# Optimization experiments

Hardware: AMD Instinct MI355X
Metric: run time of the kernel (lower is better)

The kernel has to match this reference:

```python
import jax, jax.numpy as jnp
import numpy as np

N = 50000   # nodes
E = 300000  # edges (before self-loops)
G = 64      # graphs in batch
F = 64      # feature_dim
H = 4       # n_head
C = 64      # per-head out channels (= feature_dim)
LAT = 256   # latent_dim
NEG_SLOPE = 0.2  # PyG GATConv default


def setup_inputs() -> dict:
    key = jax.random.key(0)
    ks = jax.random.split(key, 32)
    f32 = jnp.float32

    def w(k, shape, fan_in):
        return jax.random.normal(k, shape, dtype=f32) * (1.0 / np.sqrt(fan_in))

    return {
        "building_feature": jax.random.normal(ks[0], (N, 5), dtype=f32),
        "edge_index": jax.random.randint(ks[1], (2, E), 0, N, dtype=jnp.int32),
        "batch": jnp.sort(jax.random.randint(ks[2], (N,), 0, G, dtype=jnp.int32)),
        "bf_W": w(ks[3], (5, F), 5), "bf_b": jnp.zeros((F,), f32),
        "W1": w(ks[4], (F, H * C), F), "as1": w(ks[5], (H, C), C), "ad1": w(ks[6], (H, C), C), "b1": jnp.zeros((H * C,), f32),
        "W2": w(ks[7], (H * C, H * C), H * C), "as2": w(ks[8], (H, C), C), "ad2": w(ks[9], (H, C), C), "b2": jnp.zeros((H * C,), f32),
        "W3": w(ks[10], (H * C, H * C), H * C), "as3": w(ks[11], (H, C), C), "ad3": w(ks[12], (H, C), C), "b3": jnp.zeros((H * C,), f32),
        "agg_W": w(ks[13], (F * (1 + H * 3), LAT), F * (1 + H * 3)), "agg_b": jnp.zeros((LAT,), f32),
        "mu_W": w(ks[14], (LAT, LAT), LAT), "mu_b": jnp.zeros((LAT,), f32),
        "var_W": w(ks[15], (LAT, LAT), LAT), "var_b": jnp.zeros((LAT,), f32),
    }


def _gat_conv(x, W, att_src, att_dst, bias, src, dst):
    # PyG GATConv, concat=True, add_self_loops already in src/dst.
    h = (x @ W).reshape(-1, H, C)                       # [N,H,C]
    a_s = jnp.einsum("nhc,hc->nh", h, att_src)          # [N,H]
    a_d = jnp.einsum("nhc,hc->nh", h, att_dst)
    e = jax.nn.leaky_relu(a_s[src] + a_d[dst], NEG_SLOPE)  # [E,H]
    # segment softmax over incoming edges of each dst node
    m = jax.ops.segment_max(e, dst, num_segments=N)
    p = jnp.exp(e - m[dst])
    s = jax.ops.segment_sum(p, dst, num_segments=N)
    alpha = p / s[dst]                                  # [E,H]
    out = jax.ops.segment_sum(alpha[:, :, None] * h[src], dst, num_segments=N)
    return out.reshape(-1, H * C) + bias


def reference(building_feature, edge_index, batch,
              bf_W, bf_b,
              W1, as1, ad1, b1,
              W2, as2, ad2, b2,
              W3, as3, ad3, b3,
              agg_W, agg_b, mu_W, mu_b, var_W, var_b):
    # add self-loops (PyG GATConv default add_self_loops=True)
    loops = jnp.arange(N, dtype=edge_index.dtype)
    src = jnp.concatenate([edge_index[0], loops])
    dst = jnp.concatenate([edge_index[1], loops])

    n0 = jax.nn.relu(building_feature @ bf_W + bf_b)                 # [N,F]
    n1 = jax.nn.relu(_gat_conv(n0, W1, as1, ad1, b1, src, dst))      # [N,H*C]
    n2 = jax.nn.relu(_gat_conv(n1, W2, as2, ad2, b2, src, dst))
    n3 = jax.nn.relu(_gat_conv(n2, W3, as3, ad3, b3, src, dst))

    g = jnp.concatenate([
        jax.ops.segment_max(n0, batch, num_segments=G),
        jax.ops.segment_max(n1, batch, num_segments=G),
        jax.ops.segment_max(n2, batch, num_segments=G),
        jax.ops.segment_max(n3, batch, num_segments=G),
    ], axis=1)                                                       # [G, F*(1+3H)]

    latent = g @ agg_W + agg_b
    mu = latent @ mu_W + mu_b
    log_var = latent @ var_W + var_b
    return mu, log_var
```

## Files before the change

### kernel.cpp

```cpp
#include <hip/hip_runtime.h>
#include <hip/hip_bf16.h>

#define NN 50000
#define NPAD 50048
#define EE 300000
#define ETOT (EE + NN)
#define GG 64
#define GCOLS 832
#define LATD 256
#define BM 128
#define BN 128
#define NB_SCAN 196
#define LOG2E 1.4426950408889634f

typedef unsigned short u16;
typedef short s16x8 __attribute__((ext_vector_type(8)));
typedef float f32x4 __attribute__((ext_vector_type(4)));

__device__ __forceinline__ u16 f2bf(float f) {
    union { float f; unsigned u; } v; v.f = f;
    unsigned r = v.u + 0x7FFFu + ((v.u >> 16) & 1u);
    return (u16)(r >> 16);
}
__device__ __forceinline__ float bf2f(u16 u) {
    union { unsigned u; float f; } v; v.u = ((unsigned)u) << 16;
    return v.f;
}

__global__ __launch_bounds__(256) void k_prep(const float* __restrict__ W1, const float* __restrict__ W2,
                                              const float* __restrict__ W3, u16* __restrict__ Wt1,
                                              u16* __restrict__ Wt2, u16* __restrict__ Wt3,
                                              const float* __restrict__ bf, const float* __restrict__ Wb,
                                              const float* __restrict__ bb, const int* __restrict__ batch,
                                              u16* __restrict__ n0bf, int* __restrict__ gbuf,
                                              const int* __restrict__ ei, int* __restrict__ counts,
                                              u16* __restrict__ nbf) {
    int b = blockIdx.x;
    if (b < 576) {
        int idx = b * 256 + threadIdx.x;
        if (idx < 16384) {
            int n = idx >> 6, k = idx & 63;
            Wt1[idx] = f2bf(W1[k * 256 + n]);
        } else if (idx < 81920) {
            int t = idx - 16384; int n = t >> 8, k = t & 255;
            Wt2[t] = f2bf(W2[k * 256 + n]);
        } else {
            int t = idx - 81920; int n = t >> 8, k = t & 255;
            Wt3[t] = f2bf(W3[k * 256 + n]);
        }
    } else if (b < 967) {
        int c = threadIdx.x & 63;
        int sub = threadIdx.x >> 6;
        int base = (b - 576) * 128;
        int end = min(base + 128, NN);
        float w0 = Wb[c], w1 = Wb[64 + c], w2 = Wb[128 + c], w3 = Wb[192 + c], w4 = Wb[256 + c], bb_ = bb[c];
        float mx = 0.f;
        int curg = -1;
        for (int n = base + sub; n < end; n += 4) {
            const float* r = bf + (size_t)n * 5;
            float v = bb_ + r[0] * w0 + r[1] * w1 + r[2] * w2 + r[3] * w3 + r[4] * w4;
            v = fmaxf(v, 0.f);
            n0bf[(size_t)n * 64 + c] = f2bf(v);
            int g = batch[n];
            if (g != curg) {
                if (curg >= 0) atomicMax(&gbuf[curg * GCOLS + c], __float_as_int(mx));
                mx = 0.f; curg = g;
            }
            mx = fmaxf(mx, v);
        }
        if (curg >= 0) atomicMax(&gbuf[curg * GCOLS + c], __float_as_int(mx));
    } else if (b < 2335) {
        int e = (b - 967) * 256 + threadIdx.x;
        if (e < ETOT) {
            int d = (e < EE) ? ei[EE + e] : (e - EE);
            atomicAdd(&counts[d], 1);
        }
    } else {
        u16* p0 = n0bf + (size_t)NN * 64;
        for (int i = threadIdx.x; i < (NPAD - NN) * 64; i += 256) p0[i] = 0;
        u16* p1 = nbf + (size_t)NN * 256;
        for (int i = threadIdx.x; i < (NPAD - NN) * 256; i += 256) p1[i] = 0;
    }
}

__global__ __launch_bounds__(256) void k_scan_block(const int* __restrict__ counts, int* __restrict__ scanned,
                                                    int* __restrict__ bsums, int n) {
    __shared__ int sh[256];
    int i = blockIdx.x * 256 + threadIdx.x;
    int v = (i < n) ? counts[i] : 0;
    sh[threadIdx.x] = v; __syncthreads();
    for (int d = 1; d < 256; d <<= 1) {
        int t = (threadIdx.x >= d) ? sh[threadIdx.x - d] : 0;
        __syncthreads();
        sh[threadIdx.x] += t;
        __syncthreads();
    }
    if (i < n) scanned[i] = sh[threadIdx.x] - v;
    if (threadIdx.x == 255) bsums[blockIdx.x] = sh[255];
}

__global__ __launch_bounds__(256) void k_scan_add2(const int* __restrict__ scanned, const int* __restrict__ bsums,
                                                   int* __restrict__ indptr, int* __restrict__ fill) {
    __shared__ int sh[256];
    int t = threadIdx.x;
    int v = (t < NB_SCAN) ? bsums[t] : 0;
    sh[t] = v; __syncthreads();
    for (int d = 1; d < 256; d <<= 1) {
        int u = (t >= d) ? sh[t - d] : 0;
        __syncthreads();
        sh[t] += u;
        __syncthreads();
    }
    int bix = blockIdx.x;
    int boff = (bix == 0) ? 0 : sh[bix - 1];
    int i = bix * 256 + t;
    if (i < NN) { indptr[i] = scanned[i] + boff; fill[i] = 0; }
    if (i == 0) indptr[NN] = ETOT;
}

__global__ __launch_bounds__(256) void k_fill(const int* __restrict__ ei, const int* __restrict__ indptr,
                                              int* __restrict__ fill, int* __restrict__ esrc) {
    int e = blockIdx.x * 256 + threadIdx.x;
    if (e >= ETOT) return;
    int s, d;
    if (e < EE) { s = ei[e]; d = ei[EE + e]; } else { s = d = e - EE; }
    int pos = atomicAdd(&fill[d], 1);
    esrc[indptr[d] + pos] = s;
}

__global__ __launch_bounds__(256) void k_gemm_mfma(const u16* __restrict__ A,
                                                   const u16* __restrict__ Bt,
                                                   const float* __restrict__ att_s,
                                                   const float* __restrict__ att_d,
                                                   u16* __restrict__ Hbf,
                                                   float* __restrict__ a_s,
                                                   float* __restrict__ a_d,
                                                   int K) {
    __shared__ __align__(16) u16 As[128 * 64];
    __shared__ __align__(16) u16 Bs[128 * 64];
    const int tid = threadIdx.x;
    const int lane = tid & 63;
    const int w = tid >> 6;
    const int wr = w >> 1, wc = w & 1;
    const int row0 = blockIdx.x * BM;
    const int col0 = blockIdx.y * BN;

    f32x4 acc[4][4] = {};

    for (int kt = 0; kt < K; kt += 64) {
#pragma unroll
        for (int i = 0; i < 4; ++i) {
            int u = i * 256 + tid;
            int r = u >> 3, c16 = u & 7;
            int sc = ((c16 ^ (r & 7)) << 3);
            const u16* ga = A + (size_t)(row0 + r) * K + kt + sc;
            u16* la = &As[(size_t)(i * 256 + (w << 6)) * 8];
            __builtin_amdgcn_global_load_lds((const __attribute__((address_space(1))) void*)ga,
                                             (__attribute__((address_space(3))) void*)la, 16, 0, 0);
        }
#pragma unroll
        for (int i = 0; i < 4; ++i) {
            int u = i * 256 + tid;
            int r = u >> 3, c16 = u & 7;
            int sc = ((c16 ^ (r & 7)) << 3);
            const u16* gb = Bt + (size_t)(col0 + r) * K + kt + sc;
            u16* lb = &Bs[(size_t)(i * 256 + (w << 6)) * 8];
            __builtin_amdgcn_global_load_lds((const __attribute__((address_space(1))) void*)gb,
                                             (__attribute__((address_space(3))) void*)lb, 16, 0, 0);
        }
        __syncthreads();
#pragma unroll
        for (int ks = 0; ks < 2; ++ks) {
            s16x8 af[4], bfr[4];
#pragma unroll
            for (int m = 0; m < 4; ++m) {
                int ra = wr * 64 + m * 16 + (lane & 15);
                int c16 = ks * 4 + (lane >> 4);
                int off = ra * 64 + ((c16 ^ (ra & 7)) << 3);
                af[m] = *reinterpret_cast<const s16x8*>(&As[off]);
            }
#pragma unroll
            for (int n = 0; n < 4; ++n) {
                int rb = wc * 64 + n * 16 + (lane & 15);
                int c16 = ks * 4 + (lane >> 4);
                int off = rb * 64 + ((c16 ^ (rb & 7)) << 3);
                bfr[n] = *reinterpret_cast<const s16x8*>(&Bs[off]);
            }
#pragma unroll
            for (int m = 0; m < 4; ++m)
#pragma unroll
                for (int n = 0; n < 4; ++n)
                    acc[m][n] = __builtin_amdgcn_mfma_f32_16x16x32_bf16(af[m], bfr[n], acc[m][n], 0, 0, 0);
        }
        __syncthreads();
    }

    const int head = (blockIdx.y << 1) + wc;
    float asv[4], adv[4];
#pragma unroll
    for (int n = 0; n < 4; ++n) {
        asv[n] = att_s[head * 64 + n * 16 + (lane & 15)] * LOG2E;
        adv[n] = att_d[head * 64 + n * 16 + (lane & 15)] * LOG2E;
    }
#pragma unroll
    for (int m = 0; m < 4; ++m) {
        int growb = row0 + wr * 64 + m * 16 + (lane >> 4) * 4;
#pragma unroll
        for (int j = 0; j < 4; ++j) {
            int grow = growb + j;
            u16* orow = Hbf + (size_t)grow * 256 + col0 + wc * 64 + (lane & 15);
            float vs = 0.f, vd = 0.f;
#pragma unroll
            for (int n = 0; n < 4; ++n) {
                float v = acc[m][n][j];
                orow[n * 16] = f2bf(v);
                vs += v * asv[n];
                vd += v * adv[n];
            }
            vs += __shfl_xor(vs, 1); vd += __shfl_xor(vd, 1);
            vs += __shfl_xor(vs, 2); vd += __shfl_xor(vd, 2);
            vs += __shfl_xor(vs, 4); vd += __shfl_xor(vd, 4);
            vs += __shfl_xor(vs, 8); vd += __shfl_xor(vd, 8);
            if ((lane & 15) == 0) {
                a_s[grow * 4 + head] = vs;
                a_d[grow * 4 + head] = vd;
            }
        }
    }
}

__global__ __launch_bounds__(1024) void k_agg(const u16* __restrict__ Hbf, const float* __restrict__ a_s,
                                              const float* __restrict__ a_d, const int* __restrict__ indptr,
                                              const int* __restrict__ esrc, const float* __restrict__ bias,
                                              const int* __restrict__ batch, u16* __restrict__ outbf,
                                              int* __restrict__ gbuf, int poolOff) {
    __shared__ int lpool[2][256];
    if (threadIdx.x < 512) lpool[threadIdx.x >> 8][threadIdx.x & 255] = 0;
    __syncthreads();

    const int nodeBase = blockIdx.x * 16;
    const int wv = threadIdx.x >> 6;
    const int wid = nodeBase + wv;
    const int lane = threadIdx.x & 63;
    const int h = lane >> 4;
    const int eidx = lane & 15;
    const bool active = wid < NN;

    if (active) {
        int beg = indptr[wid];
        int dcount = indptr[wid + 1] - beg;
        float ad = a_d[wid * 4 + h];
        float mx = -3.0e38f, ssum = 0.f;
        float ax = 0.f, ay = 0.f, az = 0.f, aw = 0.f;

        for (int cb = 0; cb < dcount; cb += 16) {
            int cnt = min(16, dcount - cb);
            int s = (eidx < cnt) ? esrc[beg + cb + eidx] : 0;
            float el = (eidx < cnt) ? a_s[s * 4 + h] + ad : -3.0e38f;
            el = fmaxf(el, 0.2f * el);
            float cm = el;
            cm = fmaxf(cm, __shfl_xor(cm, 1));
            cm = fmaxf(cm, __shfl_xor(cm, 2));
            cm = fmaxf(cm, __shfl_xor(cm, 4));
            cm = fmaxf(cm, __shfl_xor(cm, 8));
            float nm = fmaxf(mx, cm);
            if (__any(nm > mx)) {
                float corr = exp2f(mx - nm);
                ssum *= corr; ax *= corr; ay *= corr; az *= corr; aw *= corr;
                mx = nm;
            }
            float p = exp2f(el - mx);
            float cs = p;
            cs += __shfl_xor(cs, 1);
            cs += __shfl_xor(cs, 2);
            cs += __shfl_xor(cs, 4);
            cs += __shfl_xor(cs, 8);
            ssum += cs;
            int e2 = 0;
            for (; e2 + 2 <= cnt; e2 += 2) {
                int s0 = __shfl(s, e2), s1 = __shfl(s, e2 + 1);
                float p0 = __shfl(p, (lane & 48) | e2);
                float p1 = __shfl(p, (lane & 48) | (e2 + 1));
                const ushort4 h0 = *reinterpret_cast<const ushort4*>(Hbf + (size_t)s0 * 256 + lane * 4);
                const ushort4 h1 = *reinterpret_cast<const ushort4*>(Hbf + (size_t)s1 * 256 + lane * 4);
                ax += p0 * bf2f(h0.x) + p1 * bf2f(h1.x);
                ay += p0 * bf2f(h0.y) + p1 * bf2f(h1.y);
                az += p0 * bf2f(h0.z) + p1 * bf2f(h1.z);
                aw += p0 * bf2f(h0.w) + p1 * bf2f(h1.w);
            }
            if (e2 < cnt) {
                int s0 = __shfl(s, e2);
                float p0 = __shfl(p, (lane & 48) | e2);
                const ushort4 h0 = *reinterpret_cast<const ushort4*>(Hbf + (size_t)s0 * 256 + lane * 4);
                ax += p0 * bf2f(h0.x);
                ay += p0 * bf2f(h0.y);
                az += p0 * bf2f(h0.z);
                aw += p0 * bf2f(h0.w);
            }
        }

        float inv = 1.0f / ssum;
        const float4 bv = *reinterpret_cast<const float4*>(bias + lane * 4);
        float o0 = fmaxf(ax * inv + bv.x, 0.f);
        float o1 = fmaxf(ay * inv + bv.y, 0.f);
        float o2 = fmaxf(az * inv + bv.z, 0.f);
        float o3 = fmaxf(aw * inv + bv.w, 0.f);
        ushort4 ob; ob.x = f2bf(o0); ob.y = f2bf(o1); ob.z = f2bf(o2); ob.w = f2bf(o3);
        *reinterpret_cast<ushort4*>(outbf + (size_t)wid * 256 + lane * 4) = ob;

        int g = batch[wid];
        int g0 = batch[nodeBase];
        int slot = g - g0;
        int c4 = lane * 4;
        if (slot < 2) {
            atomicMax(&lpool[slot][c4],     __float_as_int(o0));
            atomicMax(&lpool[slot][c4 + 1], __float_as_int(o1));
            atomicMax(&lpool[slot][c4 + 2], __float_as_int(o2));
            atomicMax(&lpool[slot][c4 + 3], __float_as_int(o3));
        } else {
            int* cell = &gbuf[g * GCOLS + poolOff + c4];
            atomicMax(cell,     __float_as_int(o0));
            atomicMax(cell + 1, __float_as_int(o1));
            atomicMax(cell + 2, __float_as_int(o2));
            atomicMax(cell + 3, __float_as_int(o3));
        }
    }
    __syncthreads();
    if (threadIdx.x < 512) {
        int slot = threadIdx.x >> 8, c = threadIdx.x & 255;
        int v = lpool[slot][c];
        if (v != 0) {
            int g0 = batch[nodeBase];
            atomicMax(&gbuf[(g0 + slot) * GCOLS + poolOff + c], v);
        }
    }
}

__global__ __launch_bounds__(1024) void k_head(const int* __restrict__ gbuf,
                                               const float* __restrict__ aggW, const float* __restrict__ aggb,
                                               const float* __restrict__ muW, const float* __restrict__ mub,
                                               const float* __restrict__ varW, const float* __restrict__ varb,
                                               float* __restrict__ out) {
    __shared__ float part[4][256];
    __shared__ float lat[LATD];
    int gi = blockIdx.x;
    int j = threadIdx.x & 255, ks = threadIdx.x >> 8;
    const float* g = (const float*)gbuf + (size_t)gi * GCOLS;
    float acc = 0.f;
    int k0 = ks * 208;
    for (int k = k0; k < k0 + 208; ++k) acc += g[k] * aggW[k * 256 + j];
    part[ks][j] = acc;
    __syncthreads();
    if (ks == 0) lat[j] = part[0][j] + part[1][j] + part[2][j] + part[3][j] + aggb[j];
    __syncthreads();
    const float* W = (ks < 2) ? muW : varW;
    int kb = (ks & 1) * 128;
    float am = 0.f;
    for (int k = kb; k < kb + 128; ++k) am += lat[k] * W[k * 256 + j];
    part[ks][j] = am;
    __syncthreads();
    if (ks == 0) out[(size_t)gi * 256 + j] = part[0][j] + part[1][j] + mub[j];
    else if (ks == 1) out[(size_t)GG * 256 + (size_t)gi * 256 + j] = part[2][j] + part[3][j] + varb[j];
}

extern "C" void kernel_launch(void* const* d_in, const int* in_sizes, int n_in,
                              void* d_out, int out_size, void* d_ws, size_t ws_size,
                              hipStream_t stream) {
    const float* bf   = (const float*)d_in[0];
    const int*   ei   = (const int*)d_in[1];
    const int*   batch= (const int*)d_in[2];
    const float* bf_W = (const float*)d_in[3];
    const float* bf_b = (const float*)d_in[4];
    const float* W1   = (const float*)d_in[5];
    const float* as1  = (const float*)d_in[6];
    const float* ad1  = (const float*)d_in[7];
    const float* b1   = (const float*)d_in[8];
    const float* W2   = (const float*)d_in[9];
    const float* as2  = (const float*)d_in[10];
    const float* ad2  = (const float*)d_in[11];
    const float* b2   = (const float*)d_in[12];
    const float* W3   = (const float*)d_in[13];
    const float* as3  = (const float*)d_in[14];
    const float* ad3  = (const float*)d_in[15];
    const float* b3   = (const float*)d_in[16];
    const float* aggW = (const float*)d_in[17];
    const float* aggb = (const float*)d_in[18];
    const float* muW  = (const float*)d_in[19];
    const float* mub  = (const float*)d_in[20];
    const float* varW = (const float*)d_in[21];
    const float* varb = (const float*)d_in[22];
    float* out = (float*)d_out;

    size_t off = 0;
    auto alloc = [&](size_t bytes) -> char* {
        char* p = (char*)d_ws + off;
        off += (bytes + 255) & ~(size_t)255;
        return p;
    };
    int*   counts  = (int*)alloc((size_t)(NN + GG * GCOLS) * 4);
    int*   gbuf    = counts + NN;
    u16*   Hbf     = (u16*)alloc((size_t)NPAD * 256 * 2);
    u16*   n0bf    = (u16*)alloc((size_t)NPAD * 64 * 2);
    u16*   nbf     = (u16*)alloc((size_t)NPAD * 256 * 2);
    float* a_s     = (float*)alloc((size_t)NPAD * 4 * 4);
    float* a_d     = (float*)alloc((size_t)NPAD * 4 * 4);
    int*   scanned = (int*)alloc((size_t)NN * 4);
    int*   bsums   = (int*)alloc(256 * 4);
    int*   indptr  = (int*)alloc((size_t)(NN + 1) * 4);
    int*   fill    = (int*)alloc((size_t)NN * 4);
    int*   esrc    = (int*)alloc((size_t)(ETOT + 16) * 4);
    u16*   Wt1     = (u16*)alloc((size_t)256 * 64 * 2);
    u16*   Wt2     = (u16*)alloc((size_t)256 * 256 * 2);
    u16*   Wt3     = (u16*)alloc((size_t)256 * 256 * 2);

    hipMemsetAsync(counts, 0, (size_t)(NN + GG * GCOLS) * 4, stream);

    k_prep<<<2336, 256, 0, stream>>>(W1, W2, W3, Wt1, Wt2, Wt3,
                                     bf, bf_W, bf_b, batch, n0bf, gbuf,
                                     ei, counts, nbf);

    k_scan_block<<<NB_SCAN, 256, 0, stream>>>(counts, scanned, bsums, NN);
    k_scan_add2<<<NB_SCAN, 256, 0, stream>>>(scanned, bsums, indptr, fill);
    k_fill<<<(ETOT + 255) / 256, 256, 0, stream>>>(ei, indptr, fill, esrc);

    dim3 ggrid(NPAD / BM, 256 / BN);
    const int AB = NN / 16;

    k_gemm_mfma<<<ggrid, 256, 0, stream>>>(n0bf, Wt1, as1, ad1, Hbf, a_s, a_d, 64);
    k_agg<<<AB, 1024, 0, stream>>>(Hbf, a_s, a_d, indptr, esrc, b1, batch, nbf, gbuf, 64);

    k_gemm_mfma<<<ggrid, 256, 0, stream>>>(nbf, Wt2, as2, ad2, Hbf, a_s, a_d, 256);
    k_agg<<<AB, 1024, 0, stream>>>(Hbf, a_s, a_d, indptr, esrc, b2, batch, nbf, gbuf, 320);

    k_gemm_mfma<<<ggrid, 256, 0, stream>>>(nbf, Wt3, as3, ad3, Hbf, a_s, a_d, 256);
    k_agg<<<AB, 1024, 0, stream>>>(Hbf, a_s, a_d, indptr, esrc, b3, batch, nbf, gbuf, 576);

    k_head<<<GG, 1024, 0, stream>>>(gbuf, aggW, aggb, muW, mub, varW, varb, out);
}
```

Measured before the change: 265.4 us.

## Process two nodes per wavefront in GAT aggregation with 16-byte gathers

Rework the aggregation kernel so each 64-lane wavefront handles two destination nodes (32 lanes each), with every lane accumulating 8 channels through 16-byte bf16 loads instead of 4 channels through 8-byte loads. Edge chunks shrink to 8, and both halves loop to the larger degree of the pair so shuffles stay wave-uniform. Batch ids for the block are staged in shared memory. The aim is wider memory transactions and fewer wavefronts and instructions per node, at the cost of more registers, idle lanes when the two paired degrees differ, and a different pattern of pooling atomics.

```diff
diff --git a/kernel.cpp b/kernel.cpp
--- a/kernel.cpp
+++ b/kernel.cpp
@@ -235,26 +235,35 @@
                                               const int* __restrict__ batch, u16* __restrict__ outbf,
                                               int* __restrict__ gbuf, int poolOff) {
     __shared__ int lpool[2][256];
+    __shared__ int sb[32];
     if (threadIdx.x < 512) lpool[threadIdx.x >> 8][threadIdx.x & 255] = 0;
+    const int nodeBase = blockIdx.x * 32;
+    if (threadIdx.x < 32) {
+        int nn = nodeBase + threadIdx.x;
+        sb[threadIdx.x] = (nn < NN) ? batch[nn] : -1;
+    }
     __syncthreads();
 
-    const int nodeBase = blockIdx.x * 16;
     const int wv = threadIdx.x >> 6;
-    const int wid = nodeBase + wv;
     const int lane = threadIdx.x & 63;
-    const int h = lane >> 4;
-    const int eidx = lane & 15;
+    const int half = lane >> 5;
+    const int l5 = lane & 31;
+    const int nslot = wv * 2 + half;
+    const int wid = nodeBase + nslot;
+    const int h = l5 >> 3;
+    const int eidx = l5 & 7;
     const bool active = wid < NN;
 
     if (active) {
         int beg = indptr[wid];
         int dcount = indptr[wid + 1] - beg;
+        int dmax = max(dcount, __shfl_xor(dcount, 32));
         float ad = a_d[wid * 4 + h];
         float mx = -3.0e38f, ssum = 0.f;
-        float ax = 0.f, ay = 0.f, az = 0.f, aw = 0.f;
-
-        for (int cb = 0; cb < dcount; cb += 16) {
-            int cnt = min(16, dcount - cb);
+        float a0 = 0.f, a1 = 0.f, a2 = 0.f, a3 = 0.f, a4 = 0.f, a5 = 0.f, a6 = 0.f, a7 = 0.f;
+
+        for (int cb = 0; cb < dmax; cb += 8) {
+            int cnt = min(8, dcount - cb);
             int s = (eidx < cnt) ? esrc[beg + cb + eidx] : 0;
             float el = (eidx < cnt) ? a_s[s * 4 + h] + ad : -3.0e38f;
             el = fmaxf(el, 0.2f * el);
@@ -262,77 +271,99 @@
             cm = fmaxf(cm, __shfl_xor(cm, 1));
             cm = fmaxf(cm, __shfl_xor(cm, 2));
             cm = fmaxf(cm, __shfl_xor(cm, 4));
-            cm = fmaxf(cm, __shfl_xor(cm, 8));
             float nm = fmaxf(mx, cm);
             if (__any(nm > mx)) {
                 float corr = exp2f(mx - nm);
-                ssum *= corr; ax *= corr; ay *= corr; az *= corr; aw *= corr;
-                mx = nm;
-            }
+                ssum *= corr;
+                a0 *= corr; a1 *= corr; a2 *= corr; a3 *= corr;
+                a4 *= corr; a5 *= corr; a6 *= corr; a7 *= corr;
+            }
+            mx = nm;
             float p = exp2f(el - mx);
             float cs = p;
             cs += __shfl_xor(cs, 1);
             cs += __shfl_xor(cs, 2);
             cs += __shfl_xor(cs, 4);
-            cs += __shfl_xor(cs, 8);
             ssum += cs;
-            int e2 = 0;
-            for (; e2 + 2 <= cnt; e2 += 2) {
-                int s0 = __shfl(s, e2), s1 = __shfl(s, e2 + 1);
-                float p0 = __shfl(p, (lane & 48) | e2);
-                float p1 = __shfl(p, (lane & 48) | (e2 + 1));
-                const ushort4 h0 = *reinterpret_cast<const ushort4*>(Hbf + (size_t)s0 * 256 + lane * 4);
-                const ushort4 h1 = *reinterpret_cast<const ushort4*>(Hbf + (size_t)s1 * 256 + lane * 4);
-                ax += p0 * bf2f(h0.x) + p1 * bf2f(h1.x);
-                ay += p0 * bf2f(h0.y) + p1 * bf2f(h1.y);
-                az += p0 * bf2f(h0.z) + p1 * bf2f(h1.z);
-                aw += p0 * bf2f(h0.w) + p1 * bf2f(h1.w);
-            }
-            if (e2 < cnt) {
-                int s0 = __shfl(s, e2);
-                float p0 = __shfl(p, (lane & 48) | e2);
-                const ushort4 h0 = *reinterpret_cast<const ushort4*>(Hbf + (size_t)s0 * 256 + lane * 4);
-                ax += p0 * bf2f(h0.x);
-                ay += p0 * bf2f(h0.y);
-                az += p0 * bf2f(h0.z);
-                aw += p0 * bf2f(h0.w);
+            int hb = half << 5;
+            int k = 0;
+            for (; k + 2 <= cnt; k += 2) {
+                int sk0 = __shfl(s, hb | k);
+                int sk1 = __shfl(s, hb | (k + 1));
+                float p0 = __shfl(p, hb | (h << 3) | k);
+                float p1 = __shfl(p, hb | (h << 3) | (k + 1));
+                const s16x8 h0 = *reinterpret_cast<const s16x8*>(Hbf + (size_t)sk0 * 256 + l5 * 8);
+                const s16x8 h1 = *reinterpret_cast<const s16x8*>(Hbf + (size_t)sk1 * 256 + l5 * 8);
+                a0 += p0 * bf2f((u16)h0[0]) + p1 * bf2f((u16)h1[0]);
+                a1 += p0 * bf2f((u16)h0[1]) + p1 * bf2f((u16)h1[1]);
+                a2 += p0 * bf2f((u16)h0[2]) + p1 * bf2f((u16)h1[2]);
+                a3 += p0 * bf2f((u16)h0[3]) + p1 * bf2f((u16)h1[3]);
+                a4 += p0 * bf2f((u16)h0[4]) + p1 * bf2f((u16)h1[4]);
+                a5 += p0 * bf2f((u16)h0[5]) + p1 * bf2f((u16)h1[5]);
+                a6 += p0 * bf2f((u16)h0[6]) + p1 * bf2f((u16)h1[6]);
+                a7 += p0 * bf2f((u16)h0[7]) + p1 * bf2f((u16)h1[7]);
+            }
+            if (k < cnt) {
+                int sk0 = __shfl(s, hb | k);
+                float p0 = __shfl(p, hb | (h << 3) | k);
+                const s16x8 h0 = *reinterpret_cast<const s16x8*>(Hbf + (size_t)sk0 * 256 + l5 * 8);
+                a0 += p0 * bf2f((u16)h0[0]);
+                a1 += p0 * bf2f((u16)h0[1]);
+                a2 += p0 * bf2f((u16)h0[2]);
+                a3 += p0 * bf2f((u16)h0[3]);
+                a4 += p0 * bf2f((u16)h0[4]);
+                a5 += p0 * bf2f((u16)h0[5]);
+                a6 += p0 * bf2f((u16)h0[6]);
+                a7 += p0 * bf2f((u16)h0[7]);
             }
         }
 
         float inv = 1.0f / ssum;
-        const float4 bv = *reinterpret_cast<const float4*>(bias + lane * 4);
-        float o0 = fmaxf(ax * inv + bv.x, 0.f);
-        float o1 = fmaxf(ay * inv + bv.y, 0.f);
-        float o2 = fmaxf(az * inv + bv.z, 0.f);
-        float o3 = fmaxf(aw * inv + bv.w, 0.f);
-        ushort4 ob; ob.x = f2bf(o0); ob.y = f2bf(o1); ob.z = f2bf(o2); ob.w = f2bf(o3);
-        *reinterpret_cast<ushort4*>(outbf + (size_t)wid * 256 + lane * 4) = ob;
-
-        int g = batch[wid];
-        int g0 = batch[nodeBase];
-        int slot = g - g0;
-        int c4 = lane * 4;
+        const float4 bv0 = *reinterpret_cast<const float4*>(bias + l5 * 8);
+        const float4 bv1 = *reinterpret_cast<const float4*>(bias + l5 * 8 + 4);
+        float o0 = fmaxf(a0 * inv + bv0.x, 0.f);
+        float o1 = fmaxf(a1 * inv + bv0.y, 0.f);
+        float o2 = fmaxf(a2 * inv + bv0.z, 0.f);
+        float o3 = fmaxf(a3 * inv + bv0.w, 0.f);
+        float o4 = fmaxf(a4 * inv + bv1.x, 0.f);
+        float o5 = fmaxf(a5 * inv + bv1.y, 0.f);
+        float o6 = fmaxf(a6 * inv + bv1.z, 0.f);
+        float o7 = fmaxf(a7 * inv + bv1.w, 0.f);
+        s16x8 ob;
+        ob[0] = (short)f2bf(o0); ob[1] = (short)f2bf(o1); ob[2] = (short)f2bf(o2); ob[3] = (short)f2bf(o3);
+        ob[4] = (short)f2bf(o4); ob[5] = (short)f2bf(o5); ob[6] = (short)f2bf(o6); ob[7] = (short)f2bf(o7);
+        *reinterpret_cast<s16x8*>(outbf + (size_t)wid * 256 + l5 * 8) = ob;
+
+        int g = sb[nslot];
+        int slot = g - sb[0];
+        int c8 = l5 * 8;
         if (slot < 2) {
-            atomicMax(&lpool[slot][c4],     __float_as_int(o0));
-            atomicMax(&lpool[slot][c4 + 1], __float_as_int(o1));
-            atomicMax(&lpool[slot][c4 + 2], __float_as_int(o2));
-            atomicMax(&lpool[slot][c4 + 3], __float_as_int(o3));
+            atomicMax(&lpool[slot][c8],     __float_as_int(o0));
+            atomicMax(&lpool[slot][c8 + 1], __float_as_int(o1));
+            atomicMax(&lpool[slot][c8 + 2], __float_as_int(o2));
+            atomicMax(&lpool[slot][c8 + 3], __float_as_int(o3));
+            atomicMax(&lpool[slot][c8 + 4], __float_as_int(o4));
+            atomicMax(&lpool[slot][c8 + 5], __float_as_int(o5));
+            atomicMax(&lpool[slot][c8 + 6], __float_as_int(o6));
+            atomicMax(&lpool[slot][c8 + 7], __float_as_int(o7));
         } else {
-            int* cell = &gbuf[g * GCOLS + poolOff + c4];
+            int* cell = &gbuf[g * GCOLS + poolOff + c8];
             atomicMax(cell,     __float_as_int(o0));
             atomicMax(cell + 1, __float_as_int(o1));
             atomicMax(cell + 2, __float_as_int(o2));
             atomicMax(cell + 3, __float_as_int(o3));
+            atomicMax(cell + 4, __float_as_int(o4));
+            atomicMax(cell + 5, __float_as_int(o5));
+            atomicMax(cell + 6, __float_as_int(o6));
+            atomicMax(cell + 7, __float_as_int(o7));
         }
     }
     __syncthreads();
     if (threadIdx.x < 512) {
         int slot = threadIdx.x >> 8, c = threadIdx.x & 255;
         int v = lpool[slot][c];
-        if (v != 0) {
-            int g0 = batch[nodeBase];
-            atomicMax(&gbuf[(g0 + slot) * GCOLS + poolOff + c], v);
-        }
+        if (v != 0 && sb[0] >= 0)
+            atomicMax(&gbuf[(sb[0] + slot) * GCOLS + poolOff + c], v);
     }
 }
 
@@ -424,7 +455,7 @@
     k_fill<<<(ETOT + 255) / 256, 256, 0, stream>>>(ei, indptr, fill, esrc);
 
     dim3 ggrid(NPAD / BM, 256 / BN);
-    const int AB = NN / 16;
+    const int AB = (NN + 31) / 32;
 
     k_gemm_mfma<<<ggrid, 256, 0, stream>>>(n0bf, Wt1, as1, ad1, Hbf, a_s, a_d, 64);
     k_agg<<<AB, 1024, 0, stream>>>(Hbf, a_s, a_d, indptr, esrc, b1, batch, nbf, gbuf, 64);
```

Measured after the change: 257.9 us. -2.8%, faster.
